# Kernel optimization log

Measured on AMD Instinct MI355X. Metric: run time of the kernel, lower is better.

## Reference

```python
import jax, jax.numpy as jnp
import numpy as np


def setup_inputs() -> dict:
    key = jax.random.key(0)
    ks = jax.random.split(key, 7)
    B, T, I = 512, 1000, 64
    H, OUT = 256, 128  # nhidden, 2*latent_dim
    s_ih = 1.0 / np.sqrt(I)
    s_h = 1.0 / np.sqrt(H)
    return {
        "x": jax.random.normal(ks[0], (B, T, I), dtype=jnp.float32),
        "w_ih": jax.random.normal(ks[1], (4 * H, I), dtype=jnp.float32) * s_ih,
        "w_hh": jax.random.normal(ks[2], (4 * H, H), dtype=jnp.float32) * s_h,
        "b_ih": jax.random.normal(ks[3], (4 * H,), dtype=jnp.float32) * s_h,
        "b_hh": jax.random.normal(ks[4], (4 * H,), dtype=jnp.float32) * s_h,
        "w_out": jax.random.normal(ks[5], (OUT, H), dtype=jnp.float32) * s_h,
        "b_out": jax.random.normal(ks[6], (OUT,), dtype=jnp.float32) * s_h,
    }


def reference(x, w_ih, w_hh, b_ih, b_hh, w_out, b_out):
    # forward_sequence: run LSTMCell over timesteps in REVERSED order,
    # starting from zero state; return h2o(h) of the final (t=0) step.
    B, T, I = x.shape
    H = w_hh.shape[1]
    xs = jnp.swapaxes(x[:, ::-1, :], 0, 1)  # [T, B, I], reversed time

    def step(carry, xt):
        h, c = carry
        # PyTorch LSTMCell gate order: input, forget, cell(g), output
        gates = xt @ w_ih.T + b_ih + h @ w_hh.T + b_hh  # [B, 4H]
        i, f, g, o = jnp.split(gates, 4, axis=-1)
        c_new = jax.nn.sigmoid(f) * c + jax.nn.sigmoid(i) * jnp.tanh(g)
        h_new = jax.nn.sigmoid(o) * jnp.tanh(c_new)
        return (h_new, c_new), None

    h0 = jnp.zeros((B, H), dtype=x.dtype)
    (h_fin, _), _ = jax.lax.scan(step, (h0, h0), xs)
    out = h_fin @ w_out.T + b_out  # [B, 2*latent_dim]
    return out
```

## Files before the change

kernel.cpp:

```cpp
#include <hip/hip_runtime.h>
#include <stdint.h>
#include <stddef.h>


typedef float f32x4 __attribute__((ext_vector_type(4)));
typedef short s16x8 __attribute__((ext_vector_type(8)));

#define T_STEPS 1000
#define IN_DIM  64
#define HID     256
#define STRIDE  328
#define THREADS 512
#define BT      16
#define LOG2E   1.44269504088896340736f

__device__ __forceinline__ unsigned int f2bf(float f) {
    union { float f; unsigned int u; } a; a.f = f;
    return (a.u + 0x7FFFu + ((a.u >> 16) & 1u)) >> 16;
}
__device__ __forceinline__ float bf2f(unsigned short u) {
    union { float f; unsigned int u; } a; a.u = ((unsigned int)u) << 16;
    return a.f;
}

__global__ void prep_pack(const float* __restrict__ w_ih,
                          const float* __restrict__ w_hh,
                          unsigned short* __restrict__ wpack) {
    const int lane = threadIdx.x;
    const int fid  = blockIdx.x;
    const int c  = fid >> 6;
    const int w  = (fid >> 3) & 7;
    const int j  = fid & 7;
    const int q  = j >> 1, hp = j & 1;
    const int l15 = lane & 15, hi = lane >> 4;
    const int col = (q << 8) | (w << 5) | (hp << 4) | l15;
    const int k0  = (c << 5) + (hi << 3);
    const float scale = (q == 2) ? (2.0f * LOG2E) : (-LOG2E);
    const float* src = (c < 8) ? (w_hh + (size_t)col * HID + k0)
                               : (w_ih + (size_t)col * IN_DIM + (k0 - HID));
    const f32x4 v0 = *reinterpret_cast<const f32x4*>(src);
    const f32x4 v1 = *reinterpret_cast<const f32x4*>(src + 4);
    s16x8 v;
    #pragma unroll
    for (int e = 0; e < 4; ++e) {
        v[e]     = (short)f2bf(scale * v0[e]);
        v[e + 4] = (short)f2bf(scale * v1[e]);
    }
    *reinterpret_cast<s16x8*>(wpack + (size_t)fid * 512 + lane * 8) = v;
}

__device__ __forceinline__ s16x8 raw_frag(const float* wh, const float* wi,
                                          int c, int w, int j, int hi, int l15) {
    const int q = j >> 1, hp = j & 1;
    const int col = (q << 8) | (w << 5) | (hp << 4) | l15;
    const int k0  = (c << 5) + (hi << 3);
    const float scale = (q == 2) ? (2.0f * LOG2E) : (-LOG2E);
    const float* src = (c < 8) ? (wh + (size_t)col * HID + k0)
                               : (wi + (size_t)col * IN_DIM + (k0 - HID));
    const f32x4 v0 = *reinterpret_cast<const f32x4*>(src);
    const f32x4 v1 = *reinterpret_cast<const f32x4*>(src + 4);
    s16x8 r;
    #pragma unroll
    for (int e = 0; e < 4; ++e) {
        r[e]     = (short)f2bf(scale * v0[e]);
        r[e + 4] = (short)f2bf(scale * v1[e]);
    }
    return r;
}

template<int RAW>
__global__ __launch_bounds__(THREADS, 2)
void lstm_rec(const float* __restrict__ x,
              const float* __restrict__ w_ih,
              const float* __restrict__ w_hh,
              const float* __restrict__ b_ih,
              const float* __restrict__ b_hh,
              const float* __restrict__ w_out,
              const float* __restrict__ b_out,
              const unsigned short* __restrict__ wpack,
              float* __restrict__ out)
{
    __shared__ __align__(16) unsigned short v_lds[BT][STRIDE];

    const int tid  = threadIdx.x;
    const int lane = tid & 63;
    const int w    = tid >> 6;
    const int l15  = lane & 15;
    const int hi   = lane >> 4;
    const int b0   = blockIdx.x * BT;
    const int par  = (w ^ (w >> 2)) & 1;

    s16x8 st7[8], st8[8], st9[8];
    #pragma unroll
    for (int j = 0; j < 8; ++j) {
        if constexpr (RAW) {
            st7[j] = raw_frag(w_hh, w_ih, 7, w, j, hi, l15);
            st8[j] = raw_frag(w_hh, w_ih, 8, w, j, hi, l15);
            st9[j] = raw_frag(w_hh, w_ih, 9, w, j, hi, l15);
        } else {
            st7[j] = *reinterpret_cast<const s16x8*>(wpack + ((size_t)(7*64 + w*8 + j))*512 + (lane<<3));
            st8[j] = *reinterpret_cast<const s16x8*>(wpack + ((size_t)(8*64 + w*8 + j))*512 + (lane<<3));
            st9[j] = *reinterpret_cast<const s16x8*>(wpack + ((size_t)(9*64 + w*8 + j))*512 + (lane<<3));
        }
    }

    float bias[8];
    #pragma unroll
    for (int j = 0; j < 8; ++j) {
        const int q = j >> 1, hp = j & 1;
        const int col = (q << 8) | (w << 5) | (hp << 4) | l15;
        const float scale = (q == 2) ? (2.0f * LOG2E) : (-LOG2E);
        bias[j] = scale * (b_ih[col] + b_hh[col]);
    }

    for (int i = tid; i < BT * STRIDE; i += THREADS)
        ((unsigned short*)v_lds)[i] = 0;
    __syncthreads();

    const int xrow = tid >> 4;
    const int xk   = (tid & 15) << 2;
    const float* xptr = x + (size_t)(b0 + xrow) * T_STEPS * IN_DIM + xk;
    if (tid < 256) {
        f32x4 xv0 = *reinterpret_cast<const f32x4*>(xptr + (size_t)(T_STEPS - 1) * IN_DIM);
        unsigned int p0 = f2bf(xv0[0]) | (f2bf(xv0[1]) << 16);
        unsigned int p1 = f2bf(xv0[2]) | (f2bf(xv0[3]) << 16);
        unsigned int* d = reinterpret_cast<unsigned int*>(&v_lds[xrow][HID + xk]);
        d[0] = p0; d[1] = p1;
    }
    __syncthreads();

    const unsigned short* aL = &v_lds[l15][0];

    float cst[2][4];
    #pragma unroll
    for (int a_ = 0; a_ < 2; ++a_)
        #pragma unroll
        for (int r_ = 0; r_ < 4; ++r_) cst[a_][r_] = 0.0f;

#define AF(C) (*reinterpret_cast<const s16x8*>(aL + ((C) << 5) + (hi << 3)))

#define LOADS(BUF, C) do {                                                      \
    if constexpr (RAW) {                                                        \
        _Pragma("unroll")                                                       \
        for (int j_ = 0; j_ < 8; ++j_) BUF[j_] = raw_frag(whv, wiv, (C), w, j_, hi, l15); \
    } else {                                                                    \
        _Pragma("unroll")                                                       \
        for (int j_ = 0; j_ < 8; ++j_)                                          \
            BUF[j_] = *reinterpret_cast<const s16x8*>(wpv + ((size_t)((C)*64 + w*8 + j_))*512 + (lane<<3)); \
    } } while (0)

#define CHUNK(AFV, BUF) do {                                                    \
    _Pragma("unroll")                                                           \
    for (int j_ = 0; j_ < 8; ++j_)                                              \
        acc[j_] = __builtin_amdgcn_mfma_f32_16x16x32_bf16(AFV, BUF[j_], acc[j_], 0, 0, 0); \
    } while (0)

#define POST(P) do {                                                            \
    _Pragma("unroll")                                                           \
    for (int q_ = 0; q_ < 4; ++q_) {                                            \
        const int j_ = (q_ << 1) | (P);                                         \
        acc[j_] = __builtin_amdgcn_mfma_f32_16x16x32_bf16(a7, st7[j_], acc[j_], 0, 0, 0); \
        acc[j_] = __builtin_amdgcn_mfma_f32_16x16x32_bf16(a8, st8[j_], acc[j_], 0, 0, 0); \
        acc[j_] = __builtin_amdgcn_mfma_f32_16x16x32_bf16(a9, st9[j_], acc[j_], 0, 0, 0); \
    } } while (0)

#define EW_PHASE(HP) do {                                                       \
    const int u_ = (w << 5) + ((HP) << 4) + l15;                                \
    _Pragma("unroll")                                                           \
    for (int r_ = 0; r_ < 4; ++r_) {                                            \
        const int b_ = (hi << 2) + r_;                                          \
        const float gi = acc[0 | (HP)][r_];                                     \
        const float gf = acc[2 | (HP)][r_];                                     \
        const float gg = acc[4 | (HP)][r_];                                     \
        const float go = acc[6 | (HP)][r_];                                     \
        const float si = __builtin_amdgcn_rcpf(1.0f + exp2f(gi));               \
        const float sf = __builtin_amdgcn_rcpf(1.0f + exp2f(gf));               \
        const float so = __builtin_amdgcn_rcpf(1.0f + exp2f(go));               \
        const float tg = 1.0f - 2.0f * __builtin_amdgcn_rcpf(exp2f(gg) + 1.0f); \
        float cc = cst[(HP)][r_];                                               \
        cc = sf * cc + si * tg;                                                 \
        cst[(HP)][r_] = cc;                                                     \
        const float tc = 1.0f - 2.0f * __builtin_amdgcn_rcpf(                   \
                             exp2f(2.0f * LOG2E * cc) + 1.0f);                  \
        v_lds[b_][u_] = (unsigned short)f2bf(so * tc);                          \
    } } while (0)

    f32x4 acc[8];
    #pragma unroll 1
    for (int s = 0; s < T_STEPS; ++s) {
        uintptr_t q0 = (uintptr_t)wpack, q1 = (uintptr_t)w_hh, q2 = (uintptr_t)w_ih;
        if constexpr (RAW) { asm volatile("" : "+v"(q1), "+v"(q2)); }
        else               { asm volatile("" : "+v"(q0)); }
        const unsigned short* wpv = (const unsigned short*)q0;
        const float* whv = (const float*)q1;
        const float* wiv = (const float*)q2;
        (void)wpv; (void)whv; (void)wiv;

        int tn = T_STEPS - 2 - s; tn = (tn < 0) ? 0 : tn;
        f32x4 xv;
        if (tid < 256) xv = *reinterpret_cast<const f32x4*>(xptr + (size_t)tn * IN_DIM);

        s16x8 sb0[8], sb1[8];
        LOADS(sb0, 0); LOADS(sb1, 1);
        s16x8 a0 = AF(0), a1 = AF(1), a2 = AF(2);

        #pragma unroll
        for (int j = 0; j < 8; ++j) {
            f32x4 bb = {bias[j], bias[j], bias[j], bias[j]};
            acc[j] = bb;
        }

        CHUNK(a0, sb0); LOADS(sb0, 2);
        CHUNK(a1, sb1); LOADS(sb1, 3);
        s16x8 a3 = AF(3), a4 = AF(4);
        CHUNK(a2, sb0); LOADS(sb0, 4);
        CHUNK(a3, sb1); LOADS(sb1, 5);
        s16x8 a5 = AF(5), a6 = AF(6);
        CHUNK(a4, sb0); LOADS(sb0, 6);
        CHUNK(a5, sb1);
        s16x8 a7 = AF(7), a8 = AF(8), a9 = AF(9);
        CHUNK(a6, sb0);

        __syncthreads();

        if (par == 0) { POST(0); EW_PHASE(0); POST(1); EW_PHASE(1); }
        else          { POST(1); EW_PHASE(1); POST(0); EW_PHASE(0); }

        if (tid < 256) {
            unsigned int p0 = f2bf(xv[0]) | (f2bf(xv[1]) << 16);
            unsigned int p1 = f2bf(xv[2]) | (f2bf(xv[3]) << 16);
            unsigned int* d = reinterpret_cast<unsigned int*>(&v_lds[xrow][HID + xk]);
            d[0] = p0; d[1] = p1;
        }
        __syncthreads();
    }

    const int o  = tid & 127;
    const int bq = tid >> 7;
    #pragma unroll
    for (int rb = 0; rb < 4; ++rb) {
        const int b = bq + (rb << 2);
        float a = b_out[o];
        const float* wr = w_out + (size_t)o * HID;
        #pragma unroll 8
        for (int u = 0; u < HID; u += 4) {
            f32x4 wv = *reinterpret_cast<const f32x4*>(wr + u);
            a += wv[0] * bf2f(v_lds[b][u])     + wv[1] * bf2f(v_lds[b][u + 1])
               + wv[2] * bf2f(v_lds[b][u + 2]) + wv[3] * bf2f(v_lds[b][u + 3]);
        }
        out[(size_t)(b0 + b) * 128 + o] = a;
    }
#undef AF
#undef LOADS
#undef CHUNK
#undef POST
#undef EW_PHASE
}

extern "C" void kernel_launch(void* const* d_in, const int* in_sizes, int n_in,
                              void* d_out, int out_size, void* d_ws, size_t ws_size,
                              hipStream_t stream) {
    const float* x     = (const float*)d_in[0];
    const float* w_ih  = (const float*)d_in[1];
    const float* w_hh  = (const float*)d_in[2];
    const float* b_ih  = (const float*)d_in[3];
    const float* b_hh  = (const float*)d_in[4];
    const float* w_out = (const float*)d_in[5];
    const float* b_out = (const float*)d_in[6];
    float* out = (float*)d_out;

    const bool pack = (ws_size >= (size_t)(640 * 1024));
    if (pack) {
        unsigned short* wpack = (unsigned short*)d_ws;
        hipLaunchKernelGGL(prep_pack, dim3(640), dim3(64), 0, stream, w_ih, w_hh, wpack);
        hipLaunchKernelGGL((lstm_rec<0>), dim3(512 / BT), dim3(THREADS), 0, stream,
                           x, w_ih, w_hh, b_ih, b_hh, w_out, b_out,
                           (const unsigned short*)wpack, out);
    } else {
        hipLaunchKernelGGL((lstm_rec<1>), dim3(512 / BT), dim3(THREADS), 0, stream,
                           x, w_ih, w_hh, b_ih, b_hh, w_out, b_out,
                           (const unsigned short*)nullptr, out);
    }
}
```

Measured before the change: 5.768 ms.

## Stream all weight chunks via inline-asm loads with explicit vmcnt pipelining

```diff
diff --git a/kernel.cpp b/kernel.cpp
--- a/kernel.cpp
+++ b/kernel.cpp
@@ -9,7 +9,7 @@
 #define T_STEPS 1000
 #define IN_DIM  64
 #define HID     256
-#define STRIDE  328
+#define STRIDE  264
 #define THREADS 512
 #define BT      16
 #define LOG2E   1.44269504088896340736f
@@ -68,6 +68,19 @@
     return r;
 }
 
+#define GL4(dst, addr, IMM) \
+    asm volatile("global_load_dwordx4 %0, %1, off offset:" #IMM \
+                 : "=v"(dst) : "v"(addr))
+
+#define VMW(N) do { \
+    asm volatile("s_waitcnt vmcnt(" #N ")" ::: "memory"); \
+    __builtin_amdgcn_sched_barrier(0); } while (0)
+
+#define BAR() do { \
+    __builtin_amdgcn_sched_barrier(0); \
+    asm volatile("s_waitcnt lgkmcnt(0)\n\ts_barrier" ::: "memory"); \
+    __builtin_amdgcn_sched_barrier(0); } while (0)
+
 template<int RAW>
 __global__ __launch_bounds__(THREADS, 2)
 void lstm_rec(const float* __restrict__ x,
@@ -90,20 +103,6 @@
     const int b0   = blockIdx.x * BT;
     const int par  = (w ^ (w >> 2)) & 1;
 
-    s16x8 st7[8], st8[8], st9[8];
-    #pragma unroll
-    for (int j = 0; j < 8; ++j) {
-        if constexpr (RAW) {
-            st7[j] = raw_frag(w_hh, w_ih, 7, w, j, hi, l15);
-            st8[j] = raw_frag(w_hh, w_ih, 8, w, j, hi, l15);
-            st9[j] = raw_frag(w_hh, w_ih, 9, w, j, hi, l15);
-        } else {
-            st7[j] = *reinterpret_cast<const s16x8*>(wpack + ((size_t)(7*64 + w*8 + j))*512 + (lane<<3));
-            st8[j] = *reinterpret_cast<const s16x8*>(wpack + ((size_t)(8*64 + w*8 + j))*512 + (lane<<3));
-            st9[j] = *reinterpret_cast<const s16x8*>(wpack + ((size_t)(9*64 + w*8 + j))*512 + (lane<<3));
-        }
-    }
-
     float bias[8];
     #pragma unroll
     for (int j = 0; j < 8; ++j) {
@@ -117,19 +116,10 @@
         ((unsigned short*)v_lds)[i] = 0;
     __syncthreads();
 
-    const int xrow = tid >> 4;
-    const int xk   = (tid & 15) << 2;
-    const float* xptr = x + (size_t)(b0 + xrow) * T_STEPS * IN_DIM + xk;
-    if (tid < 256) {
-        f32x4 xv0 = *reinterpret_cast<const f32x4*>(xptr + (size_t)(T_STEPS - 1) * IN_DIM);
-        unsigned int p0 = f2bf(xv0[0]) | (f2bf(xv0[1]) << 16);
-        unsigned int p1 = f2bf(xv0[2]) | (f2bf(xv0[3]) << 16);
-        unsigned int* d = reinterpret_cast<unsigned int*>(&v_lds[xrow][HID + xk]);
-        d[0] = p0; d[1] = p1;
-    }
-    __syncthreads();
-
     const unsigned short* aL = &v_lds[l15][0];
+    const uint64_t wb = (uint64_t)wpack + ((uint64_t)w << 13) + ((uint64_t)lane << 4);
+    uint64_t xaddr = (uint64_t)x
+        + ((((uint64_t)(b0 + l15)) * T_STEPS + (T_STEPS - 1)) * IN_DIM + (hi << 3)) * 4;
 
     float cst[2][4];
     #pragma unroll
@@ -139,14 +129,29 @@
 
 #define AF(C) (*reinterpret_cast<const s16x8*>(aL + ((C) << 5) + (hi << 3)))
 
-#define LOADS(BUF, C) do {                                                      \
+#define LOADCHUNK(B, C) do {                                                    \
     if constexpr (RAW) {                                                        \
         _Pragma("unroll")                                                       \
-        for (int j_ = 0; j_ < 8; ++j_) BUF[j_] = raw_frag(whv, wiv, (C), w, j_, hi, l15); \
+        for (int j_ = 0; j_ < 8; ++j_) B[j_] = raw_frag(w_hh, w_ih, (C), w, j_, hi, l15); \
     } else {                                                                    \
-        _Pragma("unroll")                                                       \
-        for (int j_ = 0; j_ < 8; ++j_)                                          \
-            BUF[j_] = *reinterpret_cast<const s16x8*>(wpv + ((size_t)((C)*64 + w*8 + j_))*512 + (lane<<3)); \
+        const uint64_t a0_ = wb + (uint64_t)((C) * 65536);                      \
+        const uint64_t a1_ = a0_ + 4096;                                        \
+        GL4(B[0], a0_, 0);    GL4(B[1], a0_, 1024);                             \
+        GL4(B[2], a0_, 2048); GL4(B[3], a0_, 3072);                             \
+        GL4(B[4], a1_, 0);    GL4(B[5], a1_, 1024);                             \
+        GL4(B[6], a1_, 2048); GL4(B[7], a1_, 3072);                             \
+    } } while (0)
+
+#define XA_ISSUE do {                                                           \
+    if constexpr (RAW) {                                                        \
+        const float* xp_ = (const float*)xaddr;                                 \
+        xa0 = *reinterpret_cast<const f32x4*>(xp_);                             \
+        xa1 = *reinterpret_cast<const f32x4*>(xp_ + 4);                         \
+        xa2 = *reinterpret_cast<const f32x4*>(xp_ + 32);                        \
+        xa3 = *reinterpret_cast<const f32x4*>(xp_ + 36);                        \
+    } else {                                                                    \
+        GL4(xa0, xaddr, 0);   GL4(xa1, xaddr, 16);                              \
+        GL4(xa2, xaddr, 128); GL4(xa3, xaddr, 144);                             \
     } } while (0)
 
 #define CHUNK(AFV, BUF) do {                                                    \
@@ -156,13 +161,14 @@
     } while (0)
 
 #define POST(P) do {                                                            \
+    __builtin_amdgcn_s_setprio(1);                                              \
     _Pragma("unroll")                                                           \
     for (int q_ = 0; q_ < 4; ++q_) {                                            \
         const int j_ = (q_ << 1) | (P);                                         \
-        acc[j_] = __builtin_amdgcn_mfma_f32_16x16x32_bf16(a7, st7[j_], acc[j_], 0, 0, 0); \
-        acc[j_] = __builtin_amdgcn_mfma_f32_16x16x32_bf16(a8, st8[j_], acc[j_], 0, 0, 0); \
-        acc[j_] = __builtin_amdgcn_mfma_f32_16x16x32_bf16(a9, st9[j_], acc[j_], 0, 0, 0); \
-    } } while (0)
+        acc[j_] = __builtin_amdgcn_mfma_f32_16x16x32_bf16(a8, B0[j_], acc[j_], 0, 0, 0); \
+        acc[j_] = __builtin_amdgcn_mfma_f32_16x16x32_bf16(a9, B1[j_], acc[j_], 0, 0, 0); \
+    }                                                                           \
+    __builtin_amdgcn_s_setprio(0); } while (0)
 
 #define EW_PHASE(HP) do {                                                       \
     const int u_ = (w << 5) + ((HP) << 4) + l15;                                \
@@ -186,54 +192,54 @@
     } } while (0)
 
     f32x4 acc[8];
+    s16x8 B0[8], B1[8];
+
+    LOADCHUNK(B0, 0);
+    LOADCHUNK(B1, 1);
+
     #pragma unroll 1
     for (int s = 0; s < T_STEPS; ++s) {
-        uintptr_t q0 = (uintptr_t)wpack, q1 = (uintptr_t)w_hh, q2 = (uintptr_t)w_ih;
-        if constexpr (RAW) { asm volatile("" : "+v"(q1), "+v"(q2)); }
-        else               { asm volatile("" : "+v"(q0)); }
-        const unsigned short* wpv = (const unsigned short*)q0;
-        const float* whv = (const float*)q1;
-        const float* wiv = (const float*)q2;
-        (void)wpv; (void)whv; (void)wiv;
-
-        int tn = T_STEPS - 2 - s; tn = (tn < 0) ? 0 : tn;
-        f32x4 xv;
-        if (tid < 256) xv = *reinterpret_cast<const f32x4*>(xptr + (size_t)tn * IN_DIM);
-
-        s16x8 sb0[8], sb1[8];
-        LOADS(sb0, 0); LOADS(sb1, 1);
-        s16x8 a0 = AF(0), a1 = AF(1), a2 = AF(2);
-
         #pragma unroll
         for (int j = 0; j < 8; ++j) {
             f32x4 bb = {bias[j], bias[j], bias[j], bias[j]};
             acc[j] = bb;
         }
-
-        CHUNK(a0, sb0); LOADS(sb0, 2);
-        CHUNK(a1, sb1); LOADS(sb1, 3);
-        s16x8 a3 = AF(3), a4 = AF(4);
-        CHUNK(a2, sb0); LOADS(sb0, 4);
-        CHUNK(a3, sb1); LOADS(sb1, 5);
-        s16x8 a5 = AF(5), a6 = AF(6);
-        CHUNK(a4, sb0); LOADS(sb0, 6);
-        CHUNK(a5, sb1);
-        s16x8 a7 = AF(7), a8 = AF(8), a9 = AF(9);
-        CHUNK(a6, sb0);
-
-        __syncthreads();
+        s16x8 a0 = AF(0), a1 = AF(1);
+        f32x4 xa0, xa1, xa2, xa3;
+        VMW(8);  CHUNK(a0, B0); LOADCHUNK(B0, 2); s16x8 a2 = AF(2);
+        VMW(8);  CHUNK(a1, B1); LOADCHUNK(B1, 3); s16x8 a3 = AF(3);
+        VMW(8);  CHUNK(a2, B0); LOADCHUNK(B0, 4); s16x8 a4 = AF(4);
+        VMW(8);  CHUNK(a3, B1); LOADCHUNK(B1, 5); s16x8 a5 = AF(5);
+        VMW(8);  CHUNK(a4, B0); LOADCHUNK(B0, 6); s16x8 a6 = AF(6);
+        VMW(8);  CHUNK(a5, B1); LOADCHUNK(B1, 7); s16x8 a7 = AF(7);
+        VMW(8);  CHUNK(a6, B0); LOADCHUNK(B0, 8);
+        VMW(8);  CHUNK(a7, B1); XA_ISSUE; LOADCHUNK(B1, 9);
+        xaddr -= (uint64_t)(IN_DIM * 4);
+        VMW(12);
+
+        BAR();
+        VMW(8);
+        s16x8 a8, a9;
+        #pragma unroll
+        for (int e = 0; e < 4; ++e) {
+            a8[e]     = (short)f2bf(xa0[e]);
+            a8[e + 4] = (short)f2bf(xa1[e]);
+            a9[e]     = (short)f2bf(xa2[e]);
+            a9[e + 4] = (short)f2bf(xa3[e]);
+        }
+        VMW(0);
 
         if (par == 0) { POST(0); EW_PHASE(0); POST(1); EW_PHASE(1); }
         else          { POST(1); EW_PHASE(1); POST(0); EW_PHASE(0); }
 
-        if (tid < 256) {
-            unsigned int p0 = f2bf(xv[0]) | (f2bf(xv[1]) << 16);
-            unsigned int p1 = f2bf(xv[2]) | (f2bf(xv[3]) << 16);
-            unsigned int* d = reinterpret_cast<unsigned int*>(&v_lds[xrow][HID + xk]);
-            d[0] = p0; d[1] = p1;
-        }
-        __syncthreads();
-    }
+        __builtin_amdgcn_sched_barrier(0);
+        LOADCHUNK(B0, 0);
+        LOADCHUNK(B1, 1);
+        BAR();
+    }
+
+    asm volatile("s_waitcnt vmcnt(0)" ::: "memory");
+    __builtin_amdgcn_sched_barrier(0);
 
     const int o  = tid & 127;
     const int bq = tid >> 7;
@@ -251,7 +257,8 @@
         out[(size_t)(b0 + b) * 128 + o] = a;
     }
 #undef AF
-#undef LOADS
+#undef LOADCHUNK
+#undef XA_ISSUE
 #undef CHUNK
 #undef POST
 #undef EW_PHASE
```

New measurement: 6.899 ms. 1.2x slower.
